# Optimization experiments

Measured on AMD Instinct MI355X. Metric: run time of the kernel, lower is better.

## Reference

```python
import jax, jax.numpy as jnp
import numpy as np

BS, SEQ, NUM_SKILLS, DIM_S, SIZE_M = 64, 200, 4096, 256, 64

def setup_inputs():
    key = jax.random.key(0)
    ks = jax.random.split(key, 16)
    def n(k, shape, s=0.05):
        return jax.random.normal(k, shape, dtype=jnp.float32) * s
    return {
        "q": jax.random.randint(ks[0], (BS, SEQ), 0, NUM_SKILLS),
        "r": jax.random.randint(ks[1], (BS, SEQ), 0, 2),
        "k_emb": n(ks[2], (NUM_SKILLS, DIM_S)),
        "x_emb": n(ks[3], (2 * NUM_SKILLS + 1, DIM_S)),
        "Mk": n(ks[4], (SIZE_M, DIM_S)),
        "Mv0": n(ks[5], (SIZE_M, DIM_S)),
        "W_a": n(ks[6], (DIM_S, 2 * DIM_S)), "b_a": jnp.zeros((DIM_S,), jnp.float32),
        "W_e": n(ks[7], (DIM_S, DIM_S)), "b_e": jnp.zeros((DIM_S,), jnp.float32),
        "W_add": n(ks[8], (DIM_S, DIM_S)), "b_add": jnp.zeros((DIM_S,), jnp.float32),
        "W_f": n(ks[9], (DIM_S, 2 * DIM_S)), "b_f": jnp.zeros((DIM_S,), jnp.float32),
        "hx": n(ks[10], (1, DIM_S)), "cx": n(ks[11], (1, DIM_S)),
        "W_ih": n(ks[12], (4 * DIM_S, DIM_S)), "b_ih": jnp.zeros((4 * DIM_S,), jnp.float32),
        "W_hh": n(ks[13], (4 * DIM_S, DIM_S)), "b_hh": jnp.zeros((4 * DIM_S,), jnp.float32),
        "W_p": n(ks[14], (1, DIM_S)), "b_p": jnp.zeros((1,), jnp.float32),
    }

def _forward(q, r, k_emb, x_emb, Mk, Mv0, W_a, b_a, W_e, b_e, W_add, b_add,
             W_f, b_f, hx, cx, W_ih, b_ih, W_hh, b_hh, W_p, b_p):
    num_skills = k_emb.shape[0]
    bs = q.shape[0]
    k = k_emb[q]                                    # (bs, seq, d) question key embedding
    v = x_emb[q + num_skills * r]                   # (bs, seq, d) interaction embedding
    # DKVMN addressing against the static key memory Mk (precomputable for all t)
    w = jax.nn.softmax(jnp.einsum('bsd,md->bsm', k, Mk), axis=-1)
    # write control input: a_embed(cat(k, v)), then erase/add head projections
    we = jnp.einsum('bse,de->bsd', jnp.concatenate([k, v], axis=-1), W_a) + b_a
    erase = jax.nn.sigmoid(jnp.einsum('bsd,ed->bse', we, W_e) + b_e)
    add = jnp.tanh(jnp.einsum('bsd,ed->bse', we, W_add) + b_add)
    mem0 = jnp.broadcast_to(Mv0, (bs,) + Mv0.shape)  # (bs, m, d)

    def mem_step(mem, inp):
        wt, et, at = inp                             # (bs,m), (bs,d), (bs,d)
        read = jnp.einsum('bm,bmd->bd', wt, mem)     # weighted read BEFORE write
        ww = wt[:, :, None]
        mem = mem * (1.0 - ww * et[:, None, :]) + ww * at[:, None, :]
        return mem, read

    _, reads = jax.lax.scan(mem_step, mem0,
                            (w.transpose(1, 0, 2), erase.transpose(1, 0, 2), add.transpose(1, 0, 2)))
    reads = reads.transpose(1, 0, 2)                 # (bs, seq, d)
    f = jnp.tanh(jnp.einsum('bse,de->bsd', jnp.concatenate([reads, k], axis=-1), W_f) + b_f)

    def lstm_step(carry, ft):
        h, c = carry
        gates = ft @ W_ih.T + b_ih + h @ W_hh.T + b_hh
        i_g, f_g, g_g, o_g = jnp.split(gates, 4, axis=-1)  # torch LSTMCell gate order
        c = jax.nn.sigmoid(f_g) * c + jax.nn.sigmoid(i_g) * jnp.tanh(g_g)
        h = jax.nn.sigmoid(o_g) * jnp.tanh(c)
        return (h, c), h

    d = hx.shape[1]
    h0 = jnp.broadcast_to(hx, (bs, d))
    c0 = jnp.broadcast_to(cx, (bs, d))
    _, hs = jax.lax.scan(lstm_step, (h0, c0), f.transpose(1, 0, 2))
    hs = hs.transpose(1, 0, 2)                       # (bs, seq, d)
    p = jax.nn.sigmoid(jnp.einsum('bsd,od->bso', hs, W_p) + b_p)[..., 0]
    return p                                         # (bs, seq)

def reference(q, r, k_emb, x_emb, Mk, Mv0, W_a, b_a, W_e, b_e, W_add, b_add,
              W_f, b_f, hx, cx, W_ih, b_ih, W_hh, b_hh, W_p, b_p):
    return _forward(q, r, k_emb, x_emb, Mk, Mv0, W_a, b_a, W_e, b_e, W_add, b_add,
                    W_f, b_f, hx, cx, W_ih, b_ih, W_hh, b_hh, W_p, b_p)
```

## Files before the change

kernel.cpp:

```cpp
#include <hip/hip_runtime.h>
#include <hip/hip_bf16.h>

#define BS 64
#define SEQ 200
#define NSK 4096
#define DS 256
#define SM 64
#define NROWS (BS*SEQ)
#define LBLK 8

typedef __attribute__((ext_vector_type(8))) short bf16x8;
typedef __attribute__((ext_vector_type(4))) float f32x4;
typedef unsigned long long u64;

__device__ __forceinline__ float sigf(float x){ return 1.0f/(1.0f+expf(-x)); }
__device__ __forceinline__ float fast_sig(float x){ return 1.0f/(1.0f+__expf(-x)); }
__device__ __forceinline__ float fast_tanh(float x){
  float t = __expf(-2.0f*fabsf(x));
  float r = (1.0f - t)/(1.0f + t);
  return copysignf(r, x);
}
__device__ __forceinline__ short f2bf(float x){
  unsigned int u = __float_as_uint(x);
  unsigned int r = (u + 0x7fffu + ((u >> 16) & 1u)) >> 16;
  return (short)r;
}
__device__ __forceinline__ float bf2f(unsigned short s){
  return __uint_as_float(((unsigned int)s) << 16);
}

__global__ __launch_bounds__(256) void k_cvtw(
    const float* __restrict__ Wa, const float* __restrict__ We,
    const float* __restrict__ Wadd, const float* __restrict__ Wf,
    const float* __restrict__ Wih, ushort* __restrict__ out)
{
  const int bid = blockIdx.x;
  const float* src; size_t rbase; int lb;
  if      (bid < 64) { src = Wa;   rbase = 0;      lb = bid; }
  else if (bid < 96) { src = We;   rbase = 131072; lb = bid - 64; }
  else if (bid < 128){ src = Wadd; rbase = 196608; lb = bid - 96; }
  else if (bid < 192){ src = Wf;   rbase = 262144; lb = bid - 128; }
  else               { src = Wih;  rbase = 393216; lb = bid - 192; }
  const int idx = (lb*256 + threadIdx.x) * 8;
  float4 a1 = *(const float4*)(src + idx);
  float4 a2 = *(const float4*)(src + idx + 4);
  bf16x8 v;
  v[0]=f2bf(a1.x); v[1]=f2bf(a1.y); v[2]=f2bf(a1.z); v[3]=f2bf(a1.w);
  v[4]=f2bf(a2.x); v[5]=f2bf(a2.y); v[6]=f2bf(a2.z); v[7]=f2bf(a2.w);
  *(bf16x8*)(out + rbase + idx) = v;
}

__global__ __launch_bounds__(256) void k_gather_attn(
    const int* __restrict__ q, const int* __restrict__ r,
    const float* __restrict__ k_emb, const float* __restrict__ x_emb,
    const float* __restrict__ Mk,
    float* __restrict__ X2, float* __restrict__ vbuf, float* __restrict__ wbuf)
{
  __shared__ float ks[4][DS];
  const int tid = threadIdx.x;
  const int wv = tid >> 6, ln = tid & 63;
  const int row = blockIdx.x * 4 + wv;
  const int b = row / SEQ, s = row % SEQ;
  const int qi = q[b*SEQ + s];
  const int ri = r[b*SEQ + s];
  const float4* kr = (const float4*)(k_emb + (size_t)qi * DS);
  const float4* vr = (const float4*)(x_emb + ((size_t)qi + (size_t)NSK * ri) * DS);
  float4 kv = kr[ln];
  float4 vv = vr[ln];
  ((float4*)(X2 + (size_t)row*512 + DS))[ln] = kv;
  ((float4*)(vbuf + (size_t)row*DS))[ln] = vv;
  *((float4*)&ks[wv][ln*4]) = kv;
  __syncthreads();
  const float4* mkr = (const float4*)(Mk + (size_t)ln * DS);
  float a0=0.f,a1=0.f,a2=0.f,a3=0.f;
  #pragma unroll 8
  for (int d4=0; d4<DS/4; d4++){
    float4 m4 = mkr[d4];
    float4 k4 = *((const float4*)&ks[wv][d4*4]);
    a0 += m4.x*k4.x; a1 += m4.y*k4.y; a2 += m4.z*k4.z; a3 += m4.w*k4.w;
  }
  float lg = (a0+a1)+(a2+a3);
  float mx = lg;
  #pragma unroll
  for (int off=32; off; off>>=1) mx = fmaxf(mx, __shfl_xor(mx, off));
  float ex = expf(lg - mx);
  float sm = ex;
  #pragma unroll
  for (int off=32; off; off>>=1) sm += __shfl_xor(sm, off);
  wbuf[(size_t)row*SM + ln] = ex / sm;
}

template<int ACT, int ABF, int OUT, int NT>
__global__ __launch_bounds__(256) void k_gemm2(
    const void* __restrict__ A0, int lda0, int K0,
    const void* __restrict__ A1, int lda1, int K1,
    const ushort* __restrict__ W, const float* __restrict__ bias,
    const float* __restrict__ bias2,
    void* __restrict__ C, int N)
{
  const int K = K0 + K1;
  __shared__ __align__(16) char As[64*80];
  __shared__ __align__(16) char Bs[NT][64*80];
  const int tid = threadIdx.x;
  const int l = tid & 63, w = tid >> 6;
  const int m0 = blockIdx.x * 64, n0 = blockIdx.y * (64*NT);
  const int mh = w >> 1, nh = w & 1;
  const int srow = tid >> 2, sseg = tid & 3;

  f32x4 acc[NT][2][2];
  #pragma unroll
  for (int nt=0; nt<NT; nt++)
    #pragma unroll
    for (int i=0;i<2;i++)
      #pragma unroll
      for (int j=0;j<2;j++) acc[nt][i][j] = (f32x4){0.f,0.f,0.f,0.f};

  for (int k0=0; k0<K; k0+=32){
    const int kk = k0 + sseg*8;
    bf16x8 av;
    if (ABF){
      const ushort* ap = (kk < K0) ? (const ushort*)A0 + (size_t)(m0+srow)*lda0 + kk
                                   : (const ushort*)A1 + (size_t)(m0+srow)*lda1 + (kk-K0);
      av = *(const bf16x8*)ap;
    } else {
      const float* ap = (kk < K0) ? (const float*)A0 + (size_t)(m0+srow)*lda0 + kk
                                  : (const float*)A1 + (size_t)(m0+srow)*lda1 + (kk-K0);
      float4 a1 = *(const float4*)ap;
      float4 a2 = *(const float4*)(ap+4);
      av[0]=f2bf(a1.x); av[1]=f2bf(a1.y); av[2]=f2bf(a1.z); av[3]=f2bf(a1.w);
      av[4]=f2bf(a2.x); av[5]=f2bf(a2.y); av[6]=f2bf(a2.z); av[7]=f2bf(a2.w);
    }
    *(bf16x8*)(As + srow*80 + ((sseg ^ (srow&3))*16)) = av;
    #pragma unroll
    for (int nt=0; nt<NT; nt++){
      bf16x8 bv = *(const bf16x8*)(W + (size_t)(n0 + nt*64 + srow)*K + kk);
      *(bf16x8*)(Bs[nt] + srow*80 + ((sseg ^ (srow&3))*16)) = bv;
    }
    __syncthreads();
    bf16x8 af[2];
    #pragma unroll
    for (int mi=0; mi<2; mi++){
      const int row = mh*32 + mi*16 + (l&15);
      af[mi] = *(const bf16x8*)(As + row*80 + (((l>>4) ^ (row&3))*16));
    }
    #pragma unroll
    for (int nt=0; nt<NT; nt++){
      bf16x8 bf[2];
      #pragma unroll
      for (int ni=0; ni<2; ni++){
        const int row = nh*32 + ni*16 + (l&15);
        bf[ni] = *(const bf16x8*)(Bs[nt] + row*80 + (((l>>4) ^ (row&3))*16));
      }
      #pragma unroll
      for (int mi=0; mi<2; mi++)
        #pragma unroll
        for (int ni=0; ni<2; ni++)
          acc[nt][mi][ni] = __builtin_amdgcn_mfma_f32_16x16x32_bf16(af[mi], bf[ni], acc[nt][mi][ni], 0,0,0);
    }
    __syncthreads();
  }
  #pragma unroll
  for (int nt=0; nt<NT; nt++){
    #pragma unroll
    for (int mi=0; mi<2; mi++){
      #pragma unroll
      for (int ni=0; ni<2; ni++){
        const int n = n0 + nt*64 + nh*32 + ni*16 + (l&15);
        float bsum = bias[n] + (bias2 ? bias2[n] : 0.f);
        #pragma unroll
        for (int j=0;j<4;j++){
          const int m = m0 + mh*32 + mi*16 + (l>>4)*4 + j;
          float v = acc[nt][mi][ni][j] + bsum;
          if (ACT==1) v = sigf(v);
          else if (ACT==2) v = tanhf(v);
          if (OUT==0)      ((float*)C)[(size_t)m*N + n] = v;
          else if (OUT==1) ((ushort*)C)[(size_t)m*N + n] = (ushort)f2bf(v);
          else             ((ushort*)C)[(size_t)m*N + ((n&255)*4 + (n>>8))] = (ushort)f2bf(v);
        }
      }
    }
  }
}

__global__ __launch_bounds__(256) void k_gemm_ea(
    const ushort* __restrict__ A, const ushort* __restrict__ We_bf,
    const float* __restrict__ b_e, const ushort* __restrict__ Wadd_bf,
    const float* __restrict__ b_add,
    float* __restrict__ ebuf, float* __restrict__ abuf)
{
  __shared__ __align__(16) char As[64*80];
  __shared__ __align__(16) char Bse[64*80];
  __shared__ __align__(16) char Bsa[64*80];
  const int tid = threadIdx.x;
  const int l = tid & 63, w = tid >> 6;
  const int m0 = blockIdx.x * 64, n0 = blockIdx.y * 64;
  const int mh = w >> 1, nh = w & 1;
  const int srow = tid >> 2, sseg = tid & 3;

  f32x4 acce[2][2], acca[2][2];
  #pragma unroll
  for (int i=0;i<2;i++)
    #pragma unroll
    for (int j=0;j<2;j++){ acce[i][j]=(f32x4){0.f,0.f,0.f,0.f}; acca[i][j]=(f32x4){0.f,0.f,0.f,0.f}; }

  for (int k0=0; k0<DS; k0+=32){
    const int kk = k0 + sseg*8;
    bf16x8 av = *(const bf16x8*)(A + (size_t)(m0+srow)*DS + kk);
    *(bf16x8*)(As + srow*80 + ((sseg ^ (srow&3))*16)) = av;
    bf16x8 be = *(const bf16x8*)(We_bf + (size_t)(n0+srow)*DS + kk);
    *(bf16x8*)(Bse + srow*80 + ((sseg ^ (srow&3))*16)) = be;
    bf16x8 ba = *(const bf16x8*)(Wadd_bf + (size_t)(n0+srow)*DS + kk);
    *(bf16x8*)(Bsa + srow*80 + ((sseg ^ (srow&3))*16)) = ba;
    __syncthreads();
    bf16x8 af[2], bfe[2], bfa[2];
    #pragma unroll
    for (int mi=0; mi<2; mi++){
      const int row = mh*32 + mi*16 + (l&15);
      af[mi] = *(const bf16x8*)(As + row*80 + (((l>>4) ^ (row&3))*16));
    }
    #pragma unroll
    for (int ni=0; ni<2; ni++){
      const int row = nh*32 + ni*16 + (l&15);
      bfe[ni] = *(const bf16x8*)(Bse + row*80 + (((l>>4) ^ (row&3))*16));
      bfa[ni] = *(const bf16x8*)(Bsa + row*80 + (((l>>4) ^ (row&3))*16));
    }
    #pragma unroll
    for (int mi=0; mi<2; mi++)
      #pragma unroll
      for (int ni=0; ni<2; ni++){
        acce[mi][ni] = __builtin_amdgcn_mfma_f32_16x16x32_bf16(af[mi], bfe[ni], acce[mi][ni], 0,0,0);
        acca[mi][ni] = __builtin_amdgcn_mfma_f32_16x16x32_bf16(af[mi], bfa[ni], acca[mi][ni], 0,0,0);
      }
    __syncthreads();
  }
  #pragma unroll
  for (int mi=0; mi<2; mi++){
    #pragma unroll
    for (int ni=0; ni<2; ni++){
      const int n = n0 + nh*32 + ni*16 + (l&15);
      const float be = b_e[n], ba = b_add[n];
      #pragma unroll
      for (int j=0;j<4;j++){
        const int m = m0 + mh*32 + mi*16 + (l>>4)*4 + j;
        ebuf[(size_t)m*DS + n] = sigf(acce[mi][ni][j] + be);
        abuf[(size_t)m*DS + n] = tanhf(acca[mi][ni][j] + ba);
      }
    }
  }
}

__global__ __launch_bounds__(256) void k_scan(
    const float* __restrict__ wbuf, const float* __restrict__ ebuf,
    const float* __restrict__ abuf, const float* __restrict__ Mv0,
    float* __restrict__ X2)
{
  const int b = blockIdx.x;
  const int d = threadIdx.x;
  __shared__ float ws[SM];
  float mem[SM];
  #pragma unroll
  for (int m=0;m<SM;m++) mem[m] = Mv0[m*DS + d];
  const size_t rb = (size_t)b*SEQ;
  float wn = (d < SM) ? wbuf[rb*SM + d] : 0.f;
  float en = ebuf[rb*DS + d];
  float an = abuf[rb*DS + d];
  for (int t=0;t<SEQ;t++){
    if (d < SM) ws[d] = wn;
    const float e = en, a = an;
    __syncthreads();
    if (t+1 < SEQ){
      wn = (d < SM) ? wbuf[(rb+t+1)*SM + d] : 0.f;
      en = ebuf[(rb+t+1)*DS + d];
      an = abuf[(rb+t+1)*DS + d];
    }
    float r0=0.f,r1=0.f,r2=0.f,r3=0.f;
    #pragma unroll
    for (int m=0;m<SM;m+=4){
      float w0=ws[m], w1=ws[m+1], w2=ws[m+2], w3=ws[m+3];
      r0 += w0*mem[m];   mem[m]   += w0*fmaf(-e, mem[m],   a);
      r1 += w1*mem[m+1]; mem[m+1] += w1*fmaf(-e, mem[m+1], a);
      r2 += w2*mem[m+2]; mem[m+2] += w2*fmaf(-e, mem[m+2], a);
      r3 += w3*mem[m+3]; mem[m+3] += w3*fmaf(-e, mem[m+3], a);
    }
    X2[(rb+t)*512 + d] = (r0+r1)+(r2+r3);
    __syncthreads();
  }
}

__global__ __launch_bounds__(512, 2) void k_lstm2(
    const ushort* __restrict__ gin2, const float* __restrict__ W_hh,
    const float* __restrict__ hx, const float* __restrict__ cx,
    short* __restrict__ hhist, unsigned long long* __restrict__ xbuf)
{
  const int bb = blockIdx.x;
  const int p  = bb >> 1;
  const int ro = bb & 1;
  const int tid = threadIdx.x;
  const int l   = tid & 63;
  const int w   = tid >> 6;

  __shared__ short hsm[2][16*256];

  bf16x8 wfr[4][8];
  {
    const int col  = l & 15;
    const int krow = (l >> 4) * 8;
    #pragma unroll
    for (int gt=0; gt<4; gt++){
      const int G = gt*256 + ro*128 + w*16 + col;
      const float* wrow = W_hh + (size_t)G*256;
      #pragma unroll
      for (int kt=0; kt<8; kt++){
        const int k0 = kt*32 + krow;
        float4 wa = *(const float4*)(wrow + k0);
        float4 wb = *(const float4*)(wrow + k0 + 4);
        bf16x8 f;
        f[0]=f2bf(wa.x); f[1]=f2bf(wa.y); f[2]=f2bf(wa.z); f[3]=f2bf(wa.w);
        f[4]=f2bf(wb.x); f[5]=f2bf(wb.y); f[6]=f2bf(wb.z); f[7]=f2bf(wb.w);
        wfr[gt][kt] = f;
      }
    }
  }

  const int dhalf = w*16 + (l & 15);
  const int gdim  = ro*128 + dhalf;
  float c_[4];
  {
    float c0 = cx[gdim];
    #pragma unroll
    for (int r=0;r<4;r++) c_[r] = c0;
  }

  if (tid < 256){
    const int row = tid >> 4, seg = tid & 15;
    #pragma unroll
    for (int u=0; u<2; u++){
      const int kb = seg*32 + u*16;
      const int d0 = kb >> 1;
      float4 ha = *(const float4*)(hx + d0);
      float4 hb = *(const float4*)(hx + d0 + 4);
      bf16x8 v;
      v[0]=f2bf(ha.x); v[1]=f2bf(ha.y); v[2]=f2bf(ha.z); v[3]=f2bf(ha.w);
      v[4]=f2bf(hb.x); v[5]=f2bf(hb.y); v[6]=f2bf(hb.z); v[7]=f2bf(hb.w);
      *(bf16x8*)((char*)hsm[0] + row*512 + (kb ^ ((row&7)<<4))) = v;
    }
  }

  u64 gpre[4];
  #pragma unroll
  for (int r=0; r<4; r++){
    const int b = p*16 + (l>>4)*4 + r;
    gpre[r] = *(const u64*)(gin2 + ((size_t)(b*SEQ))*1024 + gdim*4);
  }

  unsigned long long* myslots = xbuf + (size_t)(p*2 + ro)*1024;
  unsigned long long* pslots  = xbuf + (size_t)(p*2 + (1-ro))*1024;

  for (int t=0; t<SEQ; t++){
    __syncthreads();
    const int cur = t & 1;

    f32x4 acc[4];
    #pragma unroll
    for (int gt=0; gt<4; gt++) acc[gt] = (f32x4){0.f,0.f,0.f,0.f};
    const int r0 = l & 15;
    #pragma unroll
    for (int kt=0; kt<8; kt++){
      const int kbyte = kt*64 + (l>>4)*16;
      bf16x8 a = *(const bf16x8*)((const char*)hsm[cur] + r0*512 + (kbyte ^ ((r0&7)<<4)));
      #pragma unroll
      for (int gt=0; gt<4; gt++)
        acc[gt] = __builtin_amdgcn_mfma_f32_16x16x32_bf16(a, wfr[gt][kt], acc[gt], 0,0,0);
    }

    const unsigned int tag = (unsigned int)(t + 1);
    #pragma unroll
    for (int r=0; r<4; r++){
      const int bat = (l>>4)*4 + r;
      const int b = p*16 + bat;
      const u64 gv = gpre[r];
      float iv = acc[0][r] + bf2f((unsigned short)(gv       & 0xffffu));
      float fv = acc[1][r] + bf2f((unsigned short)((gv>>16) & 0xffffu));
      float gg = acc[2][r] + bf2f((unsigned short)((gv>>32) & 0xffffu));
      float ov = acc[3][r] + bf2f((unsigned short)((gv>>48) & 0xffffu));
      float cc = fast_sig(fv)*c_[r] + fast_sig(iv)*fast_tanh(gg);
      c_[r] = cc;
      float h = fast_sig(ov)*fast_tanh(cc);
      unsigned short hb = (unsigned short)f2bf(h);
      hhist[((size_t)(b*SEQ + t))*256 + gdim] = (short)hb;
      *(short*)((char*)hsm[cur^1] + bat*512 + ((gdim*2) ^ ((bat&7)<<4))) = (short)hb;
      unsigned short nb = (unsigned short)__shfl_xor((int)hb, 1);
      if ((l & 1) == 0){
        unsigned long long v = ((unsigned long long)hb << 48)
                             | ((unsigned long long)nb << 32)
                             | (unsigned long long)tag;
        __hip_atomic_store(&myslots[bat*64 + (dhalf>>1)], v,
                           __ATOMIC_RELAXED, __HIP_MEMORY_SCOPE_AGENT);
      }
    }

    if (t == SEQ-1) break;

    #pragma unroll
    for (int r=0; r<4; r++){
      const int b = p*16 + (l>>4)*4 + r;
      gpre[r] = *(const u64*)(gin2 + ((size_t)(b*SEQ + t+1))*1024 + gdim*4);
    }

    {
      const int s0 = tid*2, s1 = tid*2 + 1;
      unsigned long long v0=0, v1=0;
      bool ok0=false, ok1=false;
      while (true){
        if (!ok0){ v0 = __hip_atomic_load(&pslots[s0], __ATOMIC_RELAXED, __HIP_MEMORY_SCOPE_AGENT);
                   ok0 = ((unsigned int)v0 == tag); }
        if (!ok1){ v1 = __hip_atomic_load(&pslots[s1], __ATOMIC_RELAXED, __HIP_MEMORY_SCOPE_AGENT);
                   ok1 = ((unsigned int)v1 == tag); }
        if (ok0 && ok1) break;
        __builtin_amdgcn_s_sleep(1);
      }
      #pragma unroll
      for (int u=0; u<2; u++){
        unsigned long long v = u ? v1 : v0;
        const int sid = u ? s1 : s0;
        const int bat = sid >> 6;
        const int dp  = sid & 63;
        const int dpart = (1-ro)*128 + dp*2;
        unsigned int wv = (unsigned int)((v >> 48) & 0xffffu)
                        | (((unsigned int)(v >> 32) & 0xffffu) << 16);
        *(unsigned int*)((char*)hsm[cur^1] + bat*512 + ((dpart*2) ^ ((bat&7)<<4))) = wv;
      }
    }
  }
}

__global__ __launch_bounds__(256) void k_pout(
    const short* __restrict__ hhist, const float* __restrict__ W_p,
    const float* __restrict__ b_p, float* __restrict__ out)
{
  const int tid = threadIdx.x;
  const int row = blockIdx.x*4 + (tid>>6);
  const int ln = tid & 63;
  ushort4 hv = ((const ushort4*)(hhist + (size_t)row*256))[ln];
  float4 wp = ((const float4*)W_p)[ln];
  float s = bf2f(hv.x)*wp.x + bf2f(hv.y)*wp.y + bf2f(hv.z)*wp.z + bf2f(hv.w)*wp.w;
  #pragma unroll
  for (int off=32; off; off>>=1) s += __shfl_xor(s, off);
  if (ln == 0) out[row] = sigf(s + b_p[0]);
}

extern "C" void kernel_launch(void* const* d_in, const int* in_sizes, int n_in,
                              void* d_out, int out_size, void* d_ws, size_t ws_size,
                              hipStream_t stream)
{
  const int*   q     = (const int*)d_in[0];
  const int*   r     = (const int*)d_in[1];
  const float* k_emb = (const float*)d_in[2];
  const float* x_emb = (const float*)d_in[3];
  const float* Mk    = (const float*)d_in[4];
  const float* Mv0   = (const float*)d_in[5];
  const float* W_a   = (const float*)d_in[6];
  const float* b_a   = (const float*)d_in[7];
  const float* W_e   = (const float*)d_in[8];
  const float* b_e   = (const float*)d_in[9];
  const float* W_add = (const float*)d_in[10];
  const float* b_add = (const float*)d_in[11];
  const float* W_f   = (const float*)d_in[12];
  const float* b_f   = (const float*)d_in[13];
  const float* hx    = (const float*)d_in[14];
  const float* cx    = (const float*)d_in[15];
  const float* W_ih  = (const float*)d_in[16];
  const float* b_ih  = (const float*)d_in[17];
  const float* W_hh  = (const float*)d_in[18];
  const float* b_hh  = (const float*)d_in[19];
  const float* W_p   = (const float*)d_in[20];
  const float* b_p   = (const float*)d_in[21];
  float* out = (float*)d_out;

  char* base = (char*)d_ws;
  float*  vbuf  = (float*)(base);
  ushort* webuf = (ushort*)(base + 13107200);
  float*  ebuf  = (float*)(base + 19660800);
  float*  abuf  = (float*)(base + 32768000);
  float*  X2    = (float*)(base + 45875200);
  float*  wbuf  = (float*)(base + 72089600);
  ushort* fbuf  = (ushort*)(base + 75366400);
  ushort* gin2  = (ushort*)(base);
  short*  hhist = (short*)fbuf;
  u64*    xbuf  = (u64*)(base + 81920000);
  ushort* wbf   = (ushort*)(base + 82000000);

  ushort* wa_bf   = wbf;
  ushort* we_bf   = wbf + 131072;
  ushort* wadd_bf = wbf + 196608;
  ushort* wf_bf   = wbf + 262144;
  ushort* wih_bf  = wbf + 393216;

  k_cvtw<<<320, 256, 0, stream>>>(W_a, W_e, W_add, W_f, W_ih, wbf);
  k_gather_attn<<<NROWS/4, 256, 0, stream>>>(q, r, k_emb, x_emb, Mk, X2, vbuf, wbuf);
  k_gemm2<0,0,1,1><<<dim3(NROWS/64, 4), 256, 0, stream>>>(X2+DS, 512, DS, vbuf, DS, DS, wa_bf, b_a, nullptr, webuf, DS);
  k_gemm_ea<<<dim3(NROWS/64, 4), 256, 0, stream>>>(webuf, we_bf, b_e, wadd_bf, b_add, ebuf, abuf);
  k_scan<<<BS, DS, 0, stream>>>(wbuf, ebuf, abuf, Mv0, X2);
  k_gemm2<2,0,1,1><<<dim3(NROWS/64, 4), 256, 0, stream>>>(X2, 512, DS, X2+DS, 512, DS, wf_bf, b_f, nullptr, fbuf, DS);
  k_gemm2<0,1,2,2><<<dim3(NROWS/64, 8), 256, 0, stream>>>(fbuf, DS, DS, fbuf, DS, 0, wih_bf, b_ih, b_hh, gin2, 1024);
  {
    const ushort* gin_c = gin2;
    void* args[] = { (void*)&gin_c, (void*)&W_hh, (void*)&hx, (void*)&cx,
                     (void*)&hhist, (void*)&xbuf };
    hipLaunchCooperativeKernel((void*)k_lstm2, dim3(LBLK), dim3(512), args, 0, stream);
  }
  k_pout<<<NROWS/4, 256, 0, stream>>>(hhist, W_p, b_p, out);
}
```

Baseline: 1.064 ms.

## Replace paired-block LSTM with single-block-per-batch-group recurrence, weights in AGPRs/LDS

The LSTM recurrence used to split each 16-batch group across two cooperating blocks that swapped hidden-state halves every timestep through global-memory atomic flags with spin waits. Now one block owns the full 1024-gate output for its 16 batches, so that cross-block exchange is gone. The larger W_hh slice is held mostly in accumulator registers through inline-asm MFMA, with the rest spilled to LDS. This cuts inter-block latency per step but halves the number of blocks to 4, doubles the MFMA work per block, and adds LDS weight reads.

```diff
diff --git a/kernel.cpp b/kernel.cpp
--- a/kernel.cpp
+++ b/kernel.cpp
@@ -7,7 +7,9 @@
 #define DS 256
 #define SM 64
 #define NROWS (BS*SEQ)
-#define LBLK 8
+#define AG_FR 56
+#define LDS_FR 8
+#define LSTM_LDS (8192 + LDS_FR*8*1024)
 
 typedef __attribute__((ext_vector_type(8))) short bf16x8;
 typedef __attribute__((ext_vector_type(4))) float f32x4;
@@ -27,6 +29,12 @@
 }
 __device__ __forceinline__ float bf2f(unsigned short s){
   return __uint_as_float(((unsigned int)s) << 16);
+}
+__device__ __forceinline__ void mfma_a(f32x4& acc, const bf16x8& a, const bf16x8& b){
+  asm("v_mfma_f32_16x16x32_bf16 %0, %1, %2, %0" : "+v"(acc) : "v"(a), "a"(b));
+}
+__device__ __forceinline__ void mfma_v(f32x4& acc, const bf16x8& a, const bf16x8& b){
+  asm("v_mfma_f32_16x16x32_bf16 %0, %1, %2, %0" : "+v"(acc) : "v"(a), "v"(b));
 }
 
 __global__ __launch_bounds__(256) void k_cvtw(
@@ -287,48 +295,45 @@
   }
 }
 
-__global__ __launch_bounds__(512, 2) void k_lstm2(
+__global__ __launch_bounds__(512) void k_lstm_nc(
     const ushort* __restrict__ gin2, const float* __restrict__ W_hh,
     const float* __restrict__ hx, const float* __restrict__ cx,
-    short* __restrict__ hhist, unsigned long long* __restrict__ xbuf)
-{
-  const int bb = blockIdx.x;
-  const int p  = bb >> 1;
-  const int ro = bb & 1;
+    short* __restrict__ hhist)
+{
+  extern __shared__ char L[];
+  char* hsm  = L;
+  char* wlds = L + 8192;
+
+  const int g = blockIdx.x;
   const int tid = threadIdx.x;
-  const int l   = tid & 63;
-  const int w   = tid >> 6;
-
-  __shared__ short hsm[2][16*256];
-
-  bf16x8 wfr[4][8];
-  {
-    const int col  = l & 15;
-    const int krow = (l >> 4) * 8;
-    #pragma unroll
-    for (int gt=0; gt<4; gt++){
-      const int G = gt*256 + ro*128 + w*16 + col;
-      const float* wrow = W_hh + (size_t)G*256;
-      #pragma unroll
-      for (int kt=0; kt<8; kt++){
-        const int k0 = kt*32 + krow;
-        float4 wa = *(const float4*)(wrow + k0);
-        float4 wb = *(const float4*)(wrow + k0 + 4);
-        bf16x8 f;
-        f[0]=f2bf(wa.x); f[1]=f2bf(wa.y); f[2]=f2bf(wa.z); f[3]=f2bf(wa.w);
-        f[4]=f2bf(wb.x); f[5]=f2bf(wb.y); f[6]=f2bf(wb.z); f[7]=f2bf(wb.w);
-        wfr[gt][kt] = f;
-      }
-    }
-  }
-
-  const int dhalf = w*16 + (l & 15);
-  const int gdim  = ro*128 + dhalf;
-  float c_[4];
-  {
-    float c0 = cx[gdim];
-    #pragma unroll
-    for (int r=0;r<4;r++) c_[r] = c0;
+  const int l = tid & 63, w = tid >> 6;
+
+  bf16x8 wv[AG_FR];
+  #pragma unroll
+  for (int nt=0; nt<8; nt++){
+    const int gt = nt >> 1, half = nt & 1;
+    const int G = gt*256 + w*32 + half*16 + (l & 15);
+    const float* wrow = W_hh + (size_t)G*256;
+    #pragma unroll
+    for (int kt=0; kt<8; kt++){
+      const int f = nt*8 + kt;
+      const int k0 = kt*32 + (l>>4)*8;
+      float4 wa = *(const float4*)(wrow + k0);
+      float4 wb = *(const float4*)(wrow + k0 + 4);
+      bf16x8 fr;
+      fr[0]=f2bf(wa.x); fr[1]=f2bf(wa.y); fr[2]=f2bf(wa.z); fr[3]=f2bf(wa.w);
+      fr[4]=f2bf(wb.x); fr[5]=f2bf(wb.y); fr[6]=f2bf(wb.z); fr[7]=f2bf(wb.w);
+      if (f < AG_FR) wv[f] = fr;
+      else *(bf16x8*)(wlds + ((w*LDS_FR + (f - AG_FR)) << 10) + l*16) = fr;
+    }
+  }
+
+  float c_[8];
+  #pragma unroll
+  for (int half=0; half<2; half++){
+    const float c0 = cx[w*32 + half*16 + (l & 15)];
+    #pragma unroll
+    for (int j=0;j<4;j++) c_[half*4+j] = c0;
   }
 
   if (tid < 256){
@@ -342,95 +347,79 @@
       bf16x8 v;
       v[0]=f2bf(ha.x); v[1]=f2bf(ha.y); v[2]=f2bf(ha.z); v[3]=f2bf(ha.w);
       v[4]=f2bf(hb.x); v[5]=f2bf(hb.y); v[6]=f2bf(hb.z); v[7]=f2bf(hb.w);
-      *(bf16x8*)((char*)hsm[0] + row*512 + (kb ^ ((row&7)<<4))) = v;
-    }
-  }
-
-  u64 gpre[4];
-  #pragma unroll
-  for (int r=0; r<4; r++){
-    const int b = p*16 + (l>>4)*4 + r;
-    gpre[r] = *(const u64*)(gin2 + ((size_t)(b*SEQ))*1024 + gdim*4);
-  }
-
-  unsigned long long* myslots = xbuf + (size_t)(p*2 + ro)*1024;
-  unsigned long long* pslots  = xbuf + (size_t)(p*2 + (1-ro))*1024;
+      *(bf16x8*)(hsm + row*512 + (kb ^ ((row&7)<<4))) = v;
+    }
+  }
+  __syncthreads();
+
+  const int b0 = g*16 + (l>>4)*4;
+  const int d0 = w*32 + (l & 15);
+  const char* gp = (const char*)gin2 + ((size_t)(b0*SEQ)*1024 + d0*4)*2;
+  char* hp = (char*)hhist + ((size_t)(b0*SEQ)*256 + d0)*2;
 
   for (int t=0; t<SEQ; t++){
-    __syncthreads();
-    const int cur = t & 1;
-
-    f32x4 acc[4];
-    #pragma unroll
-    for (int gt=0; gt<4; gt++) acc[gt] = (f32x4){0.f,0.f,0.f,0.f};
+    u64 gld[8];
+    #pragma unroll
+    for (int half=0; half<2; half++)
+      #pragma unroll
+      for (int j=0;j<4;j++)
+        gld[half*4+j] = *(const u64*)(gp + (size_t)j*(SEQ*2048) + half*128);
+
+    bf16x8 a8[8];
     const int r0 = l & 15;
     #pragma unroll
     for (int kt=0; kt<8; kt++){
       const int kbyte = kt*64 + (l>>4)*16;
-      bf16x8 a = *(const bf16x8*)((const char*)hsm[cur] + r0*512 + (kbyte ^ ((r0&7)<<4)));
-      #pragma unroll
-      for (int gt=0; gt<4; gt++)
-        acc[gt] = __builtin_amdgcn_mfma_f32_16x16x32_bf16(a, wfr[gt][kt], acc[gt], 0,0,0);
-    }
-
-    const unsigned int tag = (unsigned int)(t + 1);
-    #pragma unroll
-    for (int r=0; r<4; r++){
-      const int bat = (l>>4)*4 + r;
-      const int b = p*16 + bat;
-      const u64 gv = gpre[r];
-      float iv = acc[0][r] + bf2f((unsigned short)(gv       & 0xffffu));
-      float fv = acc[1][r] + bf2f((unsigned short)((gv>>16) & 0xffffu));
-      float gg = acc[2][r] + bf2f((unsigned short)((gv>>32) & 0xffffu));
-      float ov = acc[3][r] + bf2f((unsigned short)((gv>>48) & 0xffffu));
-      float cc = fast_sig(fv)*c_[r] + fast_sig(iv)*fast_tanh(gg);
-      c_[r] = cc;
-      float h = fast_sig(ov)*fast_tanh(cc);
-      unsigned short hb = (unsigned short)f2bf(h);
-      hhist[((size_t)(b*SEQ + t))*256 + gdim] = (short)hb;
-      *(short*)((char*)hsm[cur^1] + bat*512 + ((gdim*2) ^ ((bat&7)<<4))) = (short)hb;
-      unsigned short nb = (unsigned short)__shfl_xor((int)hb, 1);
-      if ((l & 1) == 0){
-        unsigned long long v = ((unsigned long long)hb << 48)
-                             | ((unsigned long long)nb << 32)
-                             | (unsigned long long)tag;
-        __hip_atomic_store(&myslots[bat*64 + (dhalf>>1)], v,
-                           __ATOMIC_RELAXED, __HIP_MEMORY_SCOPE_AGENT);
-      }
-    }
-
-    if (t == SEQ-1) break;
-
-    #pragma unroll
-    for (int r=0; r<4; r++){
-      const int b = p*16 + (l>>4)*4 + r;
-      gpre[r] = *(const u64*)(gin2 + ((size_t)(b*SEQ + t+1))*1024 + gdim*4);
-    }
-
-    {
-      const int s0 = tid*2, s1 = tid*2 + 1;
-      unsigned long long v0=0, v1=0;
-      bool ok0=false, ok1=false;
-      while (true){
-        if (!ok0){ v0 = __hip_atomic_load(&pslots[s0], __ATOMIC_RELAXED, __HIP_MEMORY_SCOPE_AGENT);
-                   ok0 = ((unsigned int)v0 == tag); }
-        if (!ok1){ v1 = __hip_atomic_load(&pslots[s1], __ATOMIC_RELAXED, __HIP_MEMORY_SCOPE_AGENT);
-                   ok1 = ((unsigned int)v1 == tag); }
-        if (ok0 && ok1) break;
-        __builtin_amdgcn_s_sleep(1);
-      }
-      #pragma unroll
-      for (int u=0; u<2; u++){
-        unsigned long long v = u ? v1 : v0;
-        const int sid = u ? s1 : s0;
-        const int bat = sid >> 6;
-        const int dp  = sid & 63;
-        const int dpart = (1-ro)*128 + dp*2;
-        unsigned int wv = (unsigned int)((v >> 48) & 0xffffu)
-                        | (((unsigned int)(v >> 32) & 0xffffu) << 16);
-        *(unsigned int*)((char*)hsm[cur^1] + bat*512 + ((dpart*2) ^ ((bat&7)<<4))) = wv;
-      }
-    }
+      a8[kt] = *(const bf16x8*)(hsm + r0*512 + (kbyte ^ ((r0&7)<<4)));
+    }
+
+    f32x4 acc[8];
+    #pragma unroll
+    for (int nt=0; nt<8; nt++) acc[nt] = (f32x4){0.f,0.f,0.f,0.f};
+    #pragma unroll
+    for (int kt=0; kt<8; kt++){
+      #pragma unroll
+      for (int nt=0; nt<8; nt++){
+        const int f = nt*8 + kt;
+        if (f < AG_FR){
+          mfma_a(acc[nt], a8[kt], wv[f]);
+        } else {
+          bf16x8 bfr = *(const bf16x8*)(wlds + ((w*LDS_FR + (f - AG_FR)) << 10) + l*16);
+          mfma_v(acc[nt], a8[kt], bfr);
+        }
+      }
+    }
+
+    ushort hh[8];
+    #pragma unroll
+    for (int half=0; half<2; half++){
+      #pragma unroll
+      for (int j=0;j<4;j++){
+        const u64 gv = gld[half*4+j];
+        float iv = acc[0*2+half][j] + bf2f((unsigned short)(gv       & 0xffffu));
+        float fv = acc[1*2+half][j] + bf2f((unsigned short)((gv>>16) & 0xffffu));
+        float gg = acc[2*2+half][j] + bf2f((unsigned short)((gv>>32) & 0xffffu));
+        float ov = acc[3*2+half][j] + bf2f((unsigned short)((gv>>48) & 0xffffu));
+        float cc = fast_sig(fv)*c_[half*4+j] + fast_sig(iv)*fast_tanh(gg);
+        c_[half*4+j] = cc;
+        float h = fast_sig(ov)*fast_tanh(cc);
+        ushort hb = (ushort)f2bf(h);
+        hh[half*4+j] = hb;
+        *(short*)(hp + (size_t)j*(SEQ*512) + half*32) = (short)hb;
+      }
+    }
+    gp += 2048;
+    hp += 512;
+    __syncthreads();
+    #pragma unroll
+    for (int half=0; half<2; half++)
+      #pragma unroll
+      for (int j=0;j<4;j++){
+        const int b = (l>>4)*4 + j;
+        const int d = w*32 + half*16 + (l & 15);
+        *(short*)(hsm + b*512 + ((d*2) ^ ((b&7)<<4))) = (short)hh[half*4+j];
+      }
+    __syncthreads();
   }
 }
 
@@ -487,7 +476,6 @@
   ushort* fbuf  = (ushort*)(base + 75366400);
   ushort* gin2  = (ushort*)(base);
   short*  hhist = (short*)fbuf;
-  u64*    xbuf  = (u64*)(base + 81920000);
   ushort* wbf   = (ushort*)(base + 82000000);
 
   ushort* wa_bf   = wbf;
@@ -503,11 +491,8 @@
   k_scan<<<BS, DS, 0, stream>>>(wbuf, ebuf, abuf, Mv0, X2);
   k_gemm2<2,0,1,1><<<dim3(NROWS/64, 4), 256, 0, stream>>>(X2, 512, DS, X2+DS, 512, DS, wf_bf, b_f, nullptr, fbuf, DS);
   k_gemm2<0,1,2,2><<<dim3(NROWS/64, 8), 256, 0, stream>>>(fbuf, DS, DS, fbuf, DS, 0, wih_bf, b_ih, b_hh, gin2, 1024);
-  {
-    const ushort* gin_c = gin2;
-    void* args[] = { (void*)&gin_c, (void*)&W_hh, (void*)&hx, (void*)&cx,
-                     (void*)&hhist, (void*)&xbuf };
-    hipLaunchCooperativeKernel((void*)k_lstm2, dim3(LBLK), dim3(512), args, 0, stream);
-  }
+  hipFuncSetAttribute((const void*)k_lstm_nc,
+                      hipFuncAttributeMaxDynamicSharedMemorySize, LSTM_LDS);
+  k_lstm_nc<<<4, 512, LSTM_LDS, stream>>>(gin2, W_hh, hx, cx, hhist);
   k_pout<<<NROWS/4, 256, 0, stream>>>(hhist, W_p, b_p, out);
 }
```

Result: slower. 1.590 ms (+49.3%).

## Run LSTM recurrence in one 1024-thread block per batch group, dropping cross-block exchange

Applied to the files above, without the earlier changes.

The LSTM recurrence kernel previously split each 16-batch group across two 512-thread blocks that traded half of the hidden state every timestep through global atomic slots with spin-waiting, launched cooperatively. It now uses one 1024-thread block per group, with 16 waves covering all 256 hidden dims, so the hidden state is exchanged only through shared memory and a barrier. This removes the global-memory handshake latency from each of the 200 serial steps. In exchange only 4 blocks run instead of 8, and each block's barrier spans 16 waves.

```diff
diff --git a/kernel.cpp b/kernel.cpp
--- a/kernel.cpp
+++ b/kernel.cpp
@@ -7,7 +7,6 @@
 #define DS 256
 #define SM 64
 #define NROWS (BS*SEQ)
-#define LBLK 8
 
 typedef __attribute__((ext_vector_type(8))) short bf16x8;
 typedef __attribute__((ext_vector_type(4))) float f32x4;
@@ -287,19 +286,17 @@
   }
 }
 
-__global__ __launch_bounds__(512, 2) void k_lstm2(
+__global__ __launch_bounds__(1024, 1) void k_lstm_full(
     const ushort* __restrict__ gin2, const float* __restrict__ W_hh,
     const float* __restrict__ hx, const float* __restrict__ cx,
-    short* __restrict__ hhist, unsigned long long* __restrict__ xbuf)
-{
-  const int bb = blockIdx.x;
-  const int p  = bb >> 1;
-  const int ro = bb & 1;
+    short* __restrict__ hhist)
+{
+  __shared__ short hsm[2][16*256];
+
+  const int p   = blockIdx.x;
   const int tid = threadIdx.x;
   const int l   = tid & 63;
   const int w   = tid >> 6;
-
-  __shared__ short hsm[2][16*256];
 
   bf16x8 wfr[4][8];
   {
@@ -307,7 +304,7 @@
     const int krow = (l >> 4) * 8;
     #pragma unroll
     for (int gt=0; gt<4; gt++){
-      const int G = gt*256 + ro*128 + w*16 + col;
+      const int G = gt*256 + w*16 + col;
       const float* wrow = W_hh + (size_t)G*256;
       #pragma unroll
       for (int kt=0; kt<8; kt++){
@@ -322,8 +319,7 @@
     }
   }
 
-  const int dhalf = w*16 + (l & 15);
-  const int gdim  = ro*128 + dhalf;
+  const int gdim = w*16 + (l & 15);
   float c_[4];
   {
     float c0 = cx[gdim];
@@ -353,9 +349,6 @@
     gpre[r] = *(const u64*)(gin2 + ((size_t)(b*SEQ))*1024 + gdim*4);
   }
 
-  unsigned long long* myslots = xbuf + (size_t)(p*2 + ro)*1024;
-  unsigned long long* pslots  = xbuf + (size_t)(p*2 + (1-ro))*1024;
-
   for (int t=0; t<SEQ; t++){
     __syncthreads();
     const int cur = t & 1;
@@ -373,7 +366,6 @@
         acc[gt] = __builtin_amdgcn_mfma_f32_16x16x32_bf16(a, wfr[gt][kt], acc[gt], 0,0,0);
     }
 
-    const unsigned int tag = (unsigned int)(t + 1);
     #pragma unroll
     for (int r=0; r<4; r++){
       const int bat = (l>>4)*4 + r;
@@ -389,14 +381,6 @@
       unsigned short hb = (unsigned short)f2bf(h);
       hhist[((size_t)(b*SEQ + t))*256 + gdim] = (short)hb;
       *(short*)((char*)hsm[cur^1] + bat*512 + ((gdim*2) ^ ((bat&7)<<4))) = (short)hb;
-      unsigned short nb = (unsigned short)__shfl_xor((int)hb, 1);
-      if ((l & 1) == 0){
-        unsigned long long v = ((unsigned long long)hb << 48)
-                             | ((unsigned long long)nb << 32)
-                             | (unsigned long long)tag;
-        __hip_atomic_store(&myslots[bat*64 + (dhalf>>1)], v,
-                           __ATOMIC_RELAXED, __HIP_MEMORY_SCOPE_AGENT);
-      }
     }
 
     if (t == SEQ-1) break;
@@ -405,31 +389,6 @@
     for (int r=0; r<4; r++){
       const int b = p*16 + (l>>4)*4 + r;
       gpre[r] = *(const u64*)(gin2 + ((size_t)(b*SEQ + t+1))*1024 + gdim*4);
-    }
-
-    {
-      const int s0 = tid*2, s1 = tid*2 + 1;
-      unsigned long long v0=0, v1=0;
-      bool ok0=false, ok1=false;
-      while (true){
-        if (!ok0){ v0 = __hip_atomic_load(&pslots[s0], __ATOMIC_RELAXED, __HIP_MEMORY_SCOPE_AGENT);
-                   ok0 = ((unsigned int)v0 == tag); }
-        if (!ok1){ v1 = __hip_atomic_load(&pslots[s1], __ATOMIC_RELAXED, __HIP_MEMORY_SCOPE_AGENT);
-                   ok1 = ((unsigned int)v1 == tag); }
-        if (ok0 && ok1) break;
-        __builtin_amdgcn_s_sleep(1);
-      }
-      #pragma unroll
-      for (int u=0; u<2; u++){
-        unsigned long long v = u ? v1 : v0;
-        const int sid = u ? s1 : s0;
-        const int bat = sid >> 6;
-        const int dp  = sid & 63;
-        const int dpart = (1-ro)*128 + dp*2;
-        unsigned int wv = (unsigned int)((v >> 48) & 0xffffu)
-                        | (((unsigned int)(v >> 32) & 0xffffu) << 16);
-        *(unsigned int*)((char*)hsm[cur^1] + bat*512 + ((dpart*2) ^ ((bat&7)<<4))) = wv;
-      }
     }
   }
 }
@@ -487,7 +446,6 @@
   ushort* fbuf  = (ushort*)(base + 75366400);
   ushort* gin2  = (ushort*)(base);
   short*  hhist = (short*)fbuf;
-  u64*    xbuf  = (u64*)(base + 81920000);
   ushort* wbf   = (ushort*)(base + 82000000);
 
   ushort* wa_bf   = wbf;
@@ -503,11 +461,6 @@
   k_scan<<<BS, DS, 0, stream>>>(wbuf, ebuf, abuf, Mv0, X2);
   k_gemm2<2,0,1,1><<<dim3(NROWS/64, 4), 256, 0, stream>>>(X2, 512, DS, X2+DS, 512, DS, wf_bf, b_f, nullptr, fbuf, DS);
   k_gemm2<0,1,2,2><<<dim3(NROWS/64, 8), 256, 0, stream>>>(fbuf, DS, DS, fbuf, DS, 0, wih_bf, b_ih, b_hh, gin2, 1024);
-  {
-    const ushort* gin_c = gin2;
-    void* args[] = { (void*)&gin_c, (void*)&W_hh, (void*)&hx, (void*)&cx,
-                     (void*)&hhist, (void*)&xbuf };
-    hipLaunchCooperativeKernel((void*)k_lstm2, dim3(LBLK), dim3(512), args, 0, stream);
-  }
+  k_lstm_full<<<4, 1024, 0, stream>>>(gin2, W_hh, hx, cx, hhist);
   k_pout<<<NROWS/4, 256, 0, stream>>>(hhist, W_p, b_p, out);
 }
```

Result: slower. 2.322 ms (+118.1%).
